# Optimization experiments

Measured on AMD Instinct MI355X. Metric: run time of the kernel, lower is better.

The kernel has to match this reference:

```python
import jax, jax.numpy as jnp
import numpy as np

B = 16384      # batch
N = 128        # number of DNPU nodes (experts)
I = 3          # data electrodes per node
C = 4          # control electrodes per node
E = I + C      # total electrodes = 7
H = 90         # surrogate-model hidden width
L = 3          # number of extra hidden layers


def setup_inputs() -> dict:
    key = jax.random.key(0)
    ks = jax.random.split(key, 8)
    s_in = 1.0 / np.sqrt(E)
    s_h = 1.0 / np.sqrt(H)
    return {
        "x": jax.random.normal(ks[0], (B, N * I), dtype=jnp.float32),
        "controls": jax.random.uniform(ks[1], (N, C), dtype=jnp.float32, minval=-1.2, maxval=0.6),
        "W_in": jax.random.normal(ks[2], (N, E, H), dtype=jnp.float32) * s_in,
        "b_in": jax.random.normal(ks[3], (N, H), dtype=jnp.float32) * 0.1,
        "W_hid": jax.random.normal(ks[4], (L, N, H, H), dtype=jnp.float32) * s_h,
        "b_hid": jax.random.normal(ks[5], (L, N, H), dtype=jnp.float32) * 0.1,
        "W_out": jax.random.normal(ks[6], (N, H), dtype=jnp.float32) * s_h,
        "b_out": jax.random.normal(ks[7], (N,), dtype=jnp.float32) * 0.1,
    }


def reference(x, controls, W_in, b_in, W_hid, b_hid, W_out, b_out):
    # DNPU_Layer: partition x into N chunks of I, each node merges its data
    # electrodes with its learned control voltages into a 7-electrode vector,
    # evaluates the shared surrogate MLP with per-node parameters, outputs 1
    # current per node; results are concatenated along dim 1 -> [B, N].
    b = x.shape[0]
    xd = x.reshape(b, N, I)                                   # partition_input
    ctrl = jnp.broadcast_to(controls[None], (b, N, C))        # per-node controls
    e = jnp.concatenate([xd, ctrl], axis=-1)                  # [B, N, E]
    h = jax.nn.relu(jnp.einsum('bne,neh->bnh', e, W_in) + b_in)
    for l in range(L):  # fixed small layer count
        h = jax.nn.relu(jnp.einsum('bnh,nhk->bnk', h, W_hid[l]) + b_hid[l])
    out = jnp.einsum('bnh,nh->bn', h, W_out) + b_out          # [B, N]
    return out
```

## Files before the change

kernel.cpp:

```cpp
#include <hip/hip_runtime.h>
#include <stdint.h>

namespace {
constexpr int kB  = 16384;
constexpr int kN  = 128;
constexpr int kI  = 3;
constexpr int kC  = 4;
constexpr int kH  = 90;
constexpr int kL  = 3;
constexpr int KP  = 96;
constexpr int FB_PER_NODE = 57;
constexpr int NODE_USH    = FB_PER_NODE * 512;
constexpr size_t WT_BYTES = (size_t)kN * NODE_USH * 2;
constexpr size_t WO_OFF   = WT_BYTES;
constexpr size_t XK_OFF   = WO_OFF + (size_t)kN * KP * 4;
}

typedef __attribute__((ext_vector_type(8))) short bf16x8;
typedef __attribute__((ext_vector_type(16))) float f32x16;

__device__ __forceinline__ uint32_t pack_bf16(float lo, float hi) {
#if __has_builtin(__builtin_amdgcn_cvt_pk_bf16_f32)
  auto r = __builtin_amdgcn_cvt_pk_bf16_f32(lo, hi);
  union { decltype(r) v; uint32_t u; } c; c.v = r; return c.u;
#else
  union { float f; uint32_t i; } a, b; a.f = lo; b.f = hi;
  uint32_t ua = a.i + 0x8000u;
  uint32_t ub = b.i + 0x8000u;
  return __builtin_amdgcn_perm(ub, ua, 0x07060302);
#endif
}
__device__ __forceinline__ ushort f2bf(float f) {
  union { float f; uint32_t i; } v; v.f = f;
  uint32_t u = v.i + 0x7FFFu + ((v.i >> 16) & 1u);
  return (ushort)(u >> 16);
}

__device__ __forceinline__ void pl32swap(uint32_t& a, uint32_t& b) {
#if __has_builtin(__builtin_amdgcn_permlane32_swap)
  auto r = __builtin_amdgcn_permlane32_swap(a, b, false, false);
  a = (uint32_t)r[0]; b = (uint32_t)r[1];
#else
  uint32_t sa = (uint32_t)__shfl_xor((int)a, 32);
  uint32_t sb = (uint32_t)__shfl_xor((int)b, 32);
  bool lo = (threadIdx.x & 63) < 32;
  uint32_t na = lo ? a : sb;
  uint32_t nb = lo ? sa : b;
  a = na; b = nb;
#endif
}

__device__ __forceinline__ void stage16(const ushort* g, ushort* l) {
  __builtin_amdgcn_global_load_lds(
      (const __attribute__((address_space(1))) void*)g,
      (__attribute__((address_space(3))) void*)l, 16, 0, 0);
}

__global__ __launch_bounds__(256) void prep_kernel(
    const float* __restrict__ x,
    const float* __restrict__ W_in, const float* __restrict__ b_in,
    const float* __restrict__ W_hid, const float* __restrict__ b_hid,
    const float* __restrict__ W_out, const float* __restrict__ b_out,
    ushort* __restrict__ wt, float* __restrict__ wo, ushort* __restrict__ xk)
{
  __shared__ float smem[kH * (kH + 1) + kH];
  const int tid = threadIdx.x;
  const int bid = blockIdx.x;

  if (bid < 4 * kN) {
    float* ldsw = smem;
    float* ldsb = smem + kH * (kH + 1);
    const int node  = bid & (kN - 1);
    const int layer = bid >> 7;
    const int ksrc  = (layer == 0) ? (kI + kC) : kH;
    const float* src;
    const float* bsrc;
    if (layer == 0) { src = W_in + (size_t)node * (kI + kC) * kH; bsrc = b_in + (size_t)node * kH; }
    else {
      int l = layer - 1;
      src  = W_hid + (size_t)(l * kN + node) * kH * kH;
      bsrc = b_hid + (size_t)(l * kN + node) * kH;
    }
    for (int idx = tid; idx < ksrc * kH; idx += 256)
      ldsw[(idx / kH) * (kH + 1) + (idx % kH)] = src[idx];
    if (tid < kH) ldsb[tid] = bsrc[tid];
    __syncthreads();
    ushort* dstbase = wt + (size_t)node * NODE_USH
                    + (size_t)((layer == 0) ? 0 : 3 + (layer - 1) * 18) * 512;
    const int nch = (layer == 0) ? 192 : 1152;
#pragma unroll
    for (int it = 0; it < 5; ++it) {
      int c = tid + it * 256;
      if (c < nch) {
        int fb = c >> 6, lane = c & 63;
        int ks = (layer == 0) ? 0 : fb / 3;
        int mt = (layer == 0) ? fb : fb % 3;
        int j  = mt * 32 + (lane & 31);
        int kb = ks * 16 + (lane >> 5) * 8;
        float v[8];
#pragma unroll
        for (int i = 0; i < 8; ++i) {
          int k = kb + i;
          float t = 0.f;
          if (j < kH) {
            if (k < ksrc)       t = ldsw[k * (kH + 1) + j];
            else if (k == ksrc) t = ldsb[j];
          }
          v[i] = t;
        }
        uint4 p;
        p.x = pack_bf16(v[0], v[1]); p.y = pack_bf16(v[2], v[3]);
        p.z = pack_bf16(v[4], v[5]); p.w = pack_bf16(v[6], v[7]);
        *(uint4*)&dstbase[(size_t)c * 8] = p;
      }
    }
  } else if (bid < 4 * kN + 4) {
    int base = (bid - 4 * kN) * 3072;
    for (int t = 0; t < 12; ++t) {
      int idx = base + t * 256 + tid;
      int node = idx / KP, j = idx % KP;
      float v = 0.f;
      if (j < kH)       v = W_out[node * kH + j];
      else if (j == kH) v = b_out[node];
      wo[idx] = v;
    }
  } else {
    int xb = bid - (4 * kN + 4);
    int b0 = (xb & 255) * 64;
    int c0 = (xb >> 8) * 96;
    float* lds = smem;
    for (int idx = tid; idx < 64 * 96; idx += 256) {
      int r = idx / 96, c = idx % 96;
      lds[r * 97 + c] = x[(size_t)(b0 + r) * (kN * kI) + c0 + c];
    }
    __syncthreads();
#pragma unroll
    for (int it = 0; it < 3; ++it) {
      int c = tid + it * 256;
      int nk = c >> 3, b = (c & 7) * 8;
      float v[8];
#pragma unroll
      for (int i = 0; i < 8; ++i) v[i] = lds[(b + i) * 97 + nk];
      uint4 p;
      p.x = pack_bf16(v[0], v[1]); p.y = pack_bf16(v[2], v[3]);
      p.z = pack_bf16(v[4], v[5]); p.w = pack_bf16(v[6], v[7]);
      *(uint4*)&xk[(size_t)(c0 + nk) * kB + b0 + b] = p;
    }
  }
}

__global__ __launch_bounds__(256, 6) void dnpu_kernel(
    const ushort* __restrict__ xk, const float* __restrict__ controls,
    const ushort* __restrict__ wt, const float* __restrict__ wo,
    float* __restrict__ out)
{
  __shared__ __align__(16) ushort wbuf[18 * 512];

  const int tid  = threadIdx.x;
  const int lane = tid & 63;
  const int wid  = tid >> 6;
  const int node = (int)(blockIdx.x & 127);
  const int m0   = (int)(blockIdx.x >> 7) * 128 + wid * 32;
  const int col  = lane & 31;
  const int hh   = lane >> 5;

  const ushort* wnode = wt + (size_t)node * NODE_USH;

  auto stage_hid = [&](int l) {
    const ushort* src = wnode + (size_t)(3 + l * 18) * 512;
#pragma unroll
    for (int r = 0; r < 4; ++r)
      stage16(src + (size_t)(r * 256 + wid * 64 + lane) * 8,
              wbuf + (size_t)(r * 256 + wid * 64) * 8);
    if (wid < 2)
      stage16(src + (size_t)(1024 + wid * 64 + lane) * 8,
              wbuf + (size_t)(1024 + wid * 64) * 8);
  };

  if (wid < 3)
    stage16(wnode + (size_t)(wid * 64 + lane) * 8, &wbuf[(size_t)(wid * 64) * 8]);

  const f32x16 zf = (f32x16)0.0f;

  bf16x8 b0;
  {
    const ushort cb0 = f2bf(controls[node * kC + 0]);
    const ushort cb1 = f2bf(controls[node * kC + 1]);
    const ushort cb2 = f2bf(controls[node * kC + 2]);
    const ushort cb3 = f2bf(controls[node * kC + 3]);
    const ushort* xp = xk + (size_t)node * kI * kB + m0 + col;
    union { ushort s[8]; bf16x8 v; } f;
    f.s[0] = xp[0 * kB];
    f.s[1] = xp[1 * kB];
    f.s[2] = xp[2 * kB];
    f.s[3] = cb0; f.s[4] = cb1; f.s[5] = cb2; f.s[6] = cb3;
    f.s[7] = 0x3F80;
    bf16x8 z = (bf16x8){0,0,0,0,0,0,0,0};
    b0 = hh ? z : f.v;
  }

  union BF { uint32_t u[4]; bf16x8 v; };
  BF Bc[6], Bn[6];

  auto pack_mt = [&](int mt, const f32x16& a, BF* Bout) {
    float v[16];
#pragma unroll
    for (int r = 0; r < 16; ++r) v[r] = fmaxf(a[r], 0.f);
    if (mt == 2) v[14] = (hh == 0) ? 1.0f : v[14];
    uint32_t P[8];
#pragma unroll
    for (int w = 0; w < 8; ++w) P[w] = pack_bf16(v[2 * w], v[2 * w + 1]);
    uint32_t q0 = P[0], q2 = P[2]; pl32swap(q0, q2);
    uint32_t q1 = P[1], q3 = P[3]; pl32swap(q1, q3);
    uint32_t q4 = P[4], q6 = P[6]; pl32swap(q4, q6);
    uint32_t q5 = P[5], q7 = P[7]; pl32swap(q5, q7);
    Bout[2 * mt].u[0] = q0; Bout[2 * mt].u[1] = q1;
    Bout[2 * mt].u[2] = q2; Bout[2 * mt].u[3] = q3;
    Bout[2 * mt + 1].u[0] = q4; Bout[2 * mt + 1].u[1] = q5;
    Bout[2 * mt + 1].u[2] = q6; Bout[2 * mt + 1].u[3] = q7;
  };

  auto hidden = [&](BF* Bin, BF* Bout) {
#pragma unroll
    for (int mt = 0; mt < 3; ++mt) {
      f32x16 a;
      __builtin_amdgcn_s_setprio(1);
#pragma unroll
      for (int ks = 0; ks < 6; ++ks) {
        bf16x8 afr = *(const bf16x8*)&wbuf[(size_t)(ks * 3 + mt) * 512 + lane * 8];
        a = __builtin_amdgcn_mfma_f32_32x32x16_bf16(afr, Bin[ks].v,
                                                    ks ? a : zf, 0, 0, 0);
      }
      __builtin_amdgcn_s_setprio(0);
      pack_mt(mt, a, Bout);
    }
  };

  __syncthreads();

  {
#pragma unroll
    for (int mt = 0; mt < 3; ++mt) {
      bf16x8 afr = *(const bf16x8*)&wbuf[(size_t)mt * 512 + lane * 8];
      f32x16 a = __builtin_amdgcn_mfma_f32_32x32x16_bf16(afr, b0, zf, 0, 0, 0);
      pack_mt(mt, a, Bc);
    }
  }

  __syncthreads();
  stage_hid(0);
  __syncthreads();
  hidden(Bc, Bn);

  __syncthreads();
  stage_hid(1);
  __syncthreads();
  hidden(Bn, Bc);

  __syncthreads();
  stage_hid(2);
  __syncthreads();

  {
    const float* wop = wo + node * KP;
    float s0 = 0.f;
#pragma unroll
    for (int mt = 0; mt < 3; ++mt) {
      f32x16 a;
      __builtin_amdgcn_s_setprio(1);
#pragma unroll
      for (int ks = 0; ks < 6; ++ks) {
        bf16x8 afr = *(const bf16x8*)&wbuf[(size_t)(ks * 3 + mt) * 512 + lane * 8];
        a = __builtin_amdgcn_mfma_f32_32x32x16_bf16(afr, Bc[ks].v,
                                                    ks ? a : zf, 0, 0, 0);
      }
      __builtin_amdgcn_s_setprio(0);
#pragma unroll
      for (int g = 0; g < 4; ++g) {
        float4 wf = *(const float4*)&wop[mt * 32 + g * 8 + hh * 4];
#pragma unroll
        for (int r2 = 0; r2 < 4; ++r2) {
          int r = g * 4 + r2;
          float w = (r2 == 0) ? wf.x : (r2 == 1) ? wf.y : (r2 == 2) ? wf.z : wf.w;
          float hv = fmaxf(a[r], 0.f);
          if (mt == 2 && r == 14)
            hv = (hh == 0) ? 1.0f : hv;
          s0 += hv * w;
        }
      }
    }
    s0 += __shfl_xor(s0, 32);
    if (hh == 0)
      out[(size_t)(m0 + col) * kN + node] = s0;
  }
}

extern "C" void kernel_launch(void* const* d_in, const int* in_sizes, int n_in,
                              void* d_out, int out_size, void* d_ws, size_t ws_size,
                              hipStream_t stream) {
  const float* x        = (const float*)d_in[0];
  const float* controls = (const float*)d_in[1];
  const float* W_in     = (const float*)d_in[2];
  const float* b_in     = (const float*)d_in[3];
  const float* W_hid    = (const float*)d_in[4];
  const float* b_hid    = (const float*)d_in[5];
  const float* W_out    = (const float*)d_in[6];
  const float* b_out    = (const float*)d_in[7];
  float* out = (float*)d_out;

  ushort* wt = (ushort*)d_ws;
  float*  wo = (float*)((char*)d_ws + WO_OFF);
  ushort* xk = (ushort*)((char*)d_ws + XK_OFF);

  hipLaunchKernelGGL(prep_kernel, dim3(4 * kN + 4 + 1024), dim3(256), 0, stream,
                     x, W_in, b_in, W_hid, b_hid, W_out, b_out, wt, wo, xk);

  dim3 grid((kB / 128) * kN);
  hipLaunchKernelGGL(dnpu_kernel, grid, dim3(256), 0, stream,
                     xk, controls, wt, wo, out);
}
```

Baseline: 227.6 us.

## Stage all node weights once per block and loop over batch tiles persistently

```diff
diff --git a/kernel.cpp b/kernel.cpp
--- a/kernel.cpp
+++ b/kernel.cpp
@@ -149,55 +149,37 @@
   }
 }
 
-__global__ __launch_bounds__(256, 6) void dnpu_kernel(
+__global__ __launch_bounds__(512, 4) void dnpu_kernel(
     const ushort* __restrict__ xk, const float* __restrict__ controls,
     const ushort* __restrict__ wt, const float* __restrict__ wo,
     float* __restrict__ out)
 {
-  __shared__ __align__(16) ushort wbuf[18 * 512];
-
-  const int tid  = threadIdx.x;
-  const int lane = tid & 63;
-  const int wid  = tid >> 6;
-  const int node = (int)(blockIdx.x & 127);
-  const int m0   = (int)(blockIdx.x >> 7) * 128 + wid * 32;
-  const int col  = lane & 31;
-  const int hh   = lane >> 5;
+  __shared__ __align__(16) ushort wbuf[FB_PER_NODE * 512];
+
+  const int tid   = threadIdx.x;
+  const int lane  = tid & 63;
+  const int wid   = tid >> 6;
+  const int node  = (int)(blockIdx.x & 127);
+  const int q     = (int)(blockIdx.x >> 7);
+  const int wslot = q * 8 + wid;
+  const int col   = lane & 31;
+  const int hh    = lane >> 5;
 
   const ushort* wnode = wt + (size_t)node * NODE_USH;
 
-  auto stage_hid = [&](int l) {
-    const ushort* src = wnode + (size_t)(3 + l * 18) * 512;
-#pragma unroll
-    for (int r = 0; r < 4; ++r)
-      stage16(src + (size_t)(r * 256 + wid * 64 + lane) * 8,
-              wbuf + (size_t)(r * 256 + wid * 64) * 8);
-    if (wid < 2)
-      stage16(src + (size_t)(1024 + wid * 64 + lane) * 8,
-              wbuf + (size_t)(1024 + wid * 64) * 8);
-  };
-
-  if (wid < 3)
-    stage16(wnode + (size_t)(wid * 64 + lane) * 8, &wbuf[(size_t)(wid * 64) * 8]);
+#pragma unroll
+  for (int r = 0; r < 7; ++r)
+    stage16(wnode + (size_t)(r * 512 + wid * 64 + lane) * 8,
+            wbuf + (size_t)(r * 512 + wid * 64) * 8);
+  if (wid == 0)
+    stage16(wnode + (size_t)(3584 + lane) * 8, wbuf + (size_t)3584 * 8);
 
   const f32x16 zf = (f32x16)0.0f;
 
-  bf16x8 b0;
-  {
-    const ushort cb0 = f2bf(controls[node * kC + 0]);
-    const ushort cb1 = f2bf(controls[node * kC + 1]);
-    const ushort cb2 = f2bf(controls[node * kC + 2]);
-    const ushort cb3 = f2bf(controls[node * kC + 3]);
-    const ushort* xp = xk + (size_t)node * kI * kB + m0 + col;
-    union { ushort s[8]; bf16x8 v; } f;
-    f.s[0] = xp[0 * kB];
-    f.s[1] = xp[1 * kB];
-    f.s[2] = xp[2 * kB];
-    f.s[3] = cb0; f.s[4] = cb1; f.s[5] = cb2; f.s[6] = cb3;
-    f.s[7] = 0x3F80;
-    bf16x8 z = (bf16x8){0,0,0,0,0,0,0,0};
-    b0 = hh ? z : f.v;
-  }
+  const ushort cb0 = f2bf(controls[node * kC + 0]);
+  const ushort cb1 = f2bf(controls[node * kC + 1]);
+  const ushort cb2 = f2bf(controls[node * kC + 2]);
+  const ushort cb3 = f2bf(controls[node * kC + 3]);
 
   union BF { uint32_t u[4]; bf16x8 v; };
   BF Bc[6], Bn[6];
@@ -220,14 +202,14 @@
     Bout[2 * mt + 1].u[2] = q6; Bout[2 * mt + 1].u[3] = q7;
   };
 
-  auto hidden = [&](BF* Bin, BF* Bout) {
+  auto hidden = [&](int base, BF* Bin, BF* Bout) {
 #pragma unroll
     for (int mt = 0; mt < 3; ++mt) {
       f32x16 a;
       __builtin_amdgcn_s_setprio(1);
 #pragma unroll
       for (int ks = 0; ks < 6; ++ks) {
-        bf16x8 afr = *(const bf16x8*)&wbuf[(size_t)(ks * 3 + mt) * 512 + lane * 8];
+        bf16x8 afr = *(const bf16x8*)&wbuf[(size_t)(base + (ks * 3 + mt) * 512) + lane * 8];
         a = __builtin_amdgcn_mfma_f32_32x32x16_bf16(afr, Bin[ks].v,
                                                     ks ? a : zf, 0, 0, 0);
       }
@@ -238,31 +220,38 @@
 
   __syncthreads();
 
-  {
+  const ushort* xbase = xk + (size_t)node * kI * kB + wslot * 32 + col;
+  const float*  wop   = wo + node * KP;
+
+  ushort xa = xbase[0 * kB], xb = xbase[1 * kB], xc = xbase[2 * kB];
+
+#pragma unroll 1
+  for (int t = 0; t < 16; ++t) {
+    bf16x8 b0;
+    {
+      union { ushort s[8]; bf16x8 v; } f;
+      f.s[0] = xa; f.s[1] = xb; f.s[2] = xc;
+      f.s[3] = cb0; f.s[4] = cb1; f.s[5] = cb2; f.s[6] = cb3;
+      f.s[7] = 0x3F80;
+      bf16x8 z = (bf16x8){0,0,0,0,0,0,0,0};
+      b0 = hh ? z : f.v;
+    }
+    if (t < 15) {
+      xa = xbase[(size_t)(t + 1) * 1024 + 0 * kB];
+      xb = xbase[(size_t)(t + 1) * 1024 + 1 * kB];
+      xc = xbase[(size_t)(t + 1) * 1024 + 2 * kB];
+    }
+
 #pragma unroll
     for (int mt = 0; mt < 3; ++mt) {
       bf16x8 afr = *(const bf16x8*)&wbuf[(size_t)mt * 512 + lane * 8];
       f32x16 a = __builtin_amdgcn_mfma_f32_32x32x16_bf16(afr, b0, zf, 0, 0, 0);
       pack_mt(mt, a, Bc);
     }
-  }
-
-  __syncthreads();
-  stage_hid(0);
-  __syncthreads();
-  hidden(Bc, Bn);
-
-  __syncthreads();
-  stage_hid(1);
-  __syncthreads();
-  hidden(Bn, Bc);
-
-  __syncthreads();
-  stage_hid(2);
-  __syncthreads();
-
-  {
-    const float* wop = wo + node * KP;
+
+    hidden(3 * 512, Bc, Bn);
+    hidden((3 + 18) * 512, Bn, Bc);
+
     float s0 = 0.f;
 #pragma unroll
     for (int mt = 0; mt < 3; ++mt) {
@@ -270,7 +259,7 @@
       __builtin_amdgcn_s_setprio(1);
 #pragma unroll
       for (int ks = 0; ks < 6; ++ks) {
-        bf16x8 afr = *(const bf16x8*)&wbuf[(size_t)(ks * 3 + mt) * 512 + lane * 8];
+        bf16x8 afr = *(const bf16x8*)&wbuf[(size_t)((3 + 36) * 512 + (ks * 3 + mt) * 512) + lane * 8];
         a = __builtin_amdgcn_mfma_f32_32x32x16_bf16(afr, Bc[ks].v,
                                                     ks ? a : zf, 0, 0, 0);
       }
@@ -291,7 +280,7 @@
     }
     s0 += __shfl_xor(s0, 32);
     if (hh == 0)
-      out[(size_t)(m0 + col) * kN + node] = s0;
+      out[(size_t)(t * 1024 + wslot * 32 + col) * kN + node] = s0;
   }
 }
 
@@ -315,7 +304,7 @@
   hipLaunchKernelGGL(prep_kernel, dim3(4 * kN + 4 + 1024), dim3(256), 0, stream,
                      x, W_in, b_in, W_hid, b_hid, W_out, b_out, wt, wo, xk);
 
-  dim3 grid((kB / 128) * kN);
-  hipLaunchKernelGGL(dnpu_kernel, grid, dim3(256), 0, stream,
+  dim3 grid(4 * kN);
+  hipLaunchKernelGGL(dnpu_kernel, grid, dim3(512), 0, stream,
                      xk, controls, wt, wo, out);
 }
```

New measurement: 745.1 us. 3.27x slower.
